# Optimization experiments

Measured on AMD Instinct MI355X. Metric: run time of the kernel, lower is better.

The kernel has to match this reference:

```python
import jax, jax.numpy as jnp
import numpy as np

GROUPS = 4
EPS = 1e-5


def conv1d(x, w, b):
    # x [B,Cin,NA,T], w [Cout,Cin,1,K], 'same' padding along T
    K = w.shape[-1]
    pad = (K - 1) // 2
    y = jax.lax.conv_general_dilated(x, w, (1, 1), [(0, 0), (pad, pad)],
                                     dimension_numbers=('NCHW', 'OIHW', 'NCHW'))
    return y + b[None, :, None, None]


def group_norm(x, g, b):
    B, C, H, W = x.shape
    xg = x.reshape(B, GROUPS, C // GROUPS, H, W)
    m = xg.mean((2, 3, 4), keepdims=True)
    v = xg.var((2, 3, 4), keepdims=True)
    xn = ((xg - m) * jax.lax.rsqrt(v + EPS)).reshape(B, C, H, W)
    return xn * g[None, :, None, None] + b[None, :, None, None]


def avg_pool_t(x, k):
    B, C, H, T = x.shape
    return x.reshape(B, C, H, T // k, k).mean(-1)


def branch(x, w1, b1, g1, be1, w2, b2, g2, be2):
    y = avg_pool_t(jax.nn.gelu(group_norm(conv1d(x, w1, b1), g1, be1), approximate=False), 2)
    y = avg_pool_t(jax.nn.gelu(group_norm(conv1d(y, w2, b2), g2, be2), approximate=False), 4)
    # B C NA T -> B NA (T C)
    B, C, NA, T = y.shape
    return jnp.transpose(y, (0, 2, 3, 1)).reshape(B, NA, T * C)


def rvq(feat, cbs):
    # feat [B,NA,D]; cbs [nq,V,D] -> residual vector quantization
    def step(res, cb):
        d = (res * res).sum(-1, keepdims=True) \
            - 2.0 * jnp.einsum('bnd,vd->bnv', res, cb) \
            + (cb * cb).sum(-1)              # [B,NA,V]
        idx = jnp.argmin(d, axis=-1)          # [B,NA]
        q = cb[idx]                           # gather [B,NA,D]
        return res - q, (q, idx)
    _, (qs, idxs) = jax.lax.scan(step, feat, cbs)
    return qs.sum(0), idxs                    # [B,NA,D], [nq,B,NA]


def reference(x, w11, w12, w13, w14, b1, g1, be1,
              w21, w22, w23, w24, b2, g2, be2, codebooks):
    B, N, A, T = x.shape
    xc = x.reshape(B, N * A, T)[:, None]  # [B,1,NA,T]
    feats = jnp.stack([
        branch(xc, w11, b1[0], g1[0], be1[0], w21, b2[0], g2[0], be2[0]),
        branch(xc, w12, b1[1], g1[1], be1[1], w22, b2[1], g2[1], be2[1]),
        branch(xc, w13, b1[2], g1[2], be1[2], w23, b2[2], g2[2], be2[2]),
        branch(xc, w14, b1[3], g1[3], be1[3], w24, b2[3], g2[3], be2[3]),
    ])  # [4,B,NA,D]
    quant, idxs = jax.vmap(rvq)(feats, codebooks)  # [4,B,NA,D], [4,nq,B,NA]
    # straight-through estimator
    out = feats + jax.lax.stop_gradient(quant - feats)
    return out, idxs


def setup_inputs() -> dict:
    key = jax.random.key(0)
    ks = jax.random.split(key, 16)
    C = 8
    d = {
        'x': jax.random.normal(ks[0], (8, 32, 4, 200), jnp.float32),
        'w11': jax.random.normal(ks[1], (C, 1, 1, 21), jnp.float32) * 0.1,
        'w12': jax.random.normal(ks[2], (C, 1, 1, 15), jnp.float32) * 0.1,
        'w13': jax.random.normal(ks[3], (C, 1, 1, 9), jnp.float32) * 0.1,
        'w14': jax.random.normal(ks[4], (C, 1, 1, 5), jnp.float32) * 0.1,
        'b1': jnp.zeros((4, C), jnp.float32),
        'g1': jnp.ones((4, C), jnp.float32),
        'be1': jnp.zeros((4, C), jnp.float32),
        'w21': jax.random.normal(ks[5], (C, C, 1, 9), jnp.float32) * 0.1,
        'w22': jax.random.normal(ks[6], (C, C, 1, 7), jnp.float32) * 0.1,
        'w23': jax.random.normal(ks[7], (C, C, 1, 5), jnp.float32) * 0.1,
        'w24': jax.random.normal(ks[8], (C, C, 1, 3), jnp.float32) * 0.1,
        'b2': jnp.zeros((4, C), jnp.float32),
        'g2': jnp.ones((4, C), jnp.float32),
        'be2': jnp.zeros((4, C), jnp.float32),
        'codebooks': jax.random.normal(ks[9], (4, 8, 8192, 200), jnp.float32) * 0.5,
    }
    return d
```

## Files before the change

kernel.cpp:

```cpp
#include <hip/hip_runtime.h>
#include <hip/hip_bf16.h>
#include <math.h>

#define NBR 4
#define BB 8
#define NAA 128
#define T_IN 200
#define CCH 8
#define NQ 8
#define NV 8192
#define DD 200
#define ROWS 1024
#define KPAD 224
#define NKG 28
#define CBQSH ((size_t)NBR*NKG*NV*8)

typedef __attribute__((ext_vector_type(8))) short short8;
typedef __attribute__((ext_vector_type(4))) float f32x4;

__device__ __forceinline__ unsigned short f2bf(float x) {
  unsigned u = __float_as_uint(x);
  unsigned r = (u + 0x7fffu + ((u >> 16) & 1u)) >> 16;
  return (unsigned short)r;
}
__device__ __forceinline__ bool lexlt(float av, int ai, float bv, int bi) {
  return (av < bv) || (av == bv && ai < bi);
}
__device__ __forceinline__ unsigned umn(unsigned a, unsigned b) { return a < b ? a : b; }
__device__ __forceinline__ unsigned umx(unsigned a, unsigned b) { return a > b ? a : b; }
__device__ __forceinline__ unsigned skey(float s, int idx) {
  unsigned u = __float_as_uint(s);
  unsigned mask = ((unsigned)((int)u >> 31)) | 0x80000000u;
  return ((u ^ mask) & 0xFFFFE000u) | (unsigned)idx;
}
__device__ __forceinline__ void gld16(const short* g, short* s) {
  __builtin_amdgcn_global_load_lds(
      (const __attribute__((address_space(1))) unsigned*)g,
      (__attribute__((address_space(3))) unsigned*)s, 16, 0, 0);
}

template<int K>
__device__ __forceinline__ void conv1_stats_body(
    const float* __restrict__ sx, const float* __restrict__ wr, float bias,
    int tl, double& s, double& s2)
{
  constexpr int pad = (K-1)/2;
  if (tl < 25) {
    int t0 = 8*tl;
    float xw[K+7];
    #pragma unroll
    for (int i = 0; i < K+7; ++i) {
      int xi = t0 - pad + i;
      xw[i] = ((unsigned)xi < (unsigned)T_IN) ? sx[xi] : 0.f;
    }
    #pragma unroll
    for (int m = 0; m < 8; ++m) {
      float acc = bias;
      #pragma unroll
      for (int k = 0; k < K; ++k)
        acc = fmaf(wr[k], xw[m + k], acc);
      s += acc; s2 += (double)acc * acc;
    }
  }
}

__global__ __launch_bounds__(256) void k_conv1_stats(
    const float* __restrict__ x,
    const float* __restrict__ w11, const float* __restrict__ w12,
    const float* __restrict__ w13, const float* __restrict__ w14,
    const float* __restrict__ b1,
    double* __restrict__ partS, double* __restrict__ partQ)
{
  const int bid = blockIdx.x;
  const int br = bid >> 10;
  const int b  = (bid >> 7) & 7;
  const int na = bid & 127;
  const int tid = threadIdx.x;
  const int c  = tid >> 5;
  const int tl = tid & 31;
  const float* w = (br==0) ? w11 : (br==1) ? w12 : (br==2) ? w13 : w14;

  __shared__ float sx[T_IN];
  if (tid < T_IN) sx[tid] = x[((size_t)b*NAA + na)*T_IN + tid];
  __syncthreads();

  const float bias = b1[br*CCH + c];
  double s = 0.0, s2 = 0.0;
  switch (br) {
    case 0: conv1_stats_body<21>(sx, w + c*21, bias, tl, s, s2); break;
    case 1: conv1_stats_body<15>(sx, w + c*15, bias, tl, s, s2); break;
    case 2: conv1_stats_body<9> (sx, w + c*9,  bias, tl, s, s2); break;
    default: conv1_stats_body<5>(sx, w + c*5,  bias, tl, s, s2); break;
  }
  __shared__ double rs[256], rq[256];
  rs[tid] = s; rq[tid] = s2;
  __syncthreads();
  for (int off = 32; off > 0; off >>= 1) {
    if ((tid & 63) < off) { rs[tid] += rs[tid+off]; rq[tid] += rq[tid+off]; }
    __syncthreads();
  }
  if ((tid & 63) == 0) {
    int g = tid >> 6;
    int pi = (((br*BB + b)*4 + g) << 7) + na;
    partS[pi] = rs[tid]; partQ[pi] = rq[tid];
  }
}

template<int K1, int K2>
__device__ __forceinline__ void mid_body(
    const float* __restrict__ sx, float* __restrict__ sy,
    const float* __restrict__ w1, const float* __restrict__ w2,
    float bias1, float fm, float rst, float gm, float bt, float bias2,
    int c, int tl, float* __restrict__ yout, double& s, double& s2)
{
  constexpr int pad1 = (K1-1)/2, pad2 = (K2-1)/2;
  const float* wr = w1 + c*K1;
  if (tl < 25) {
    int t0 = 8*tl;
    float xw[K1+7];
    #pragma unroll
    for (int i = 0; i < K1+7; ++i) {
      int xi = t0 - pad1 + i;
      xw[i] = ((unsigned)xi < (unsigned)T_IN) ? sx[xi] : 0.f;
    }
    #pragma unroll
    for (int m = 0; m < 4; ++m) {
      float u = 0.f;
      #pragma unroll
      for (int h = 0; h < 2; ++h) {
        float acc = bias1;
        #pragma unroll
        for (int k = 0; k < K1; ++k)
          acc = fmaf(wr[k], xw[2*m + h + k], acc);
        float xn = (acc - fm) * rst * gm + bt;
        u += 0.5f * xn * (1.0f + erff(xn * 0.70710678118654752440f));
      }
      sy[c*100 + 4*tl + m] = 0.5f * u;
    }
  }
  __syncthreads();
  if (tl < 25) {
    int t0 = 4*tl;
    float a0 = bias2, a1 = bias2, a2 = bias2, a3 = bias2;
    #pragma unroll
    for (int cin = 0; cin < CCH; ++cin) {
      const float* wr2 = w2 + (c*CCH + cin)*K2;
      float wv[K2];
      #pragma unroll
      for (int k = 0; k < K2; ++k) wv[k] = wr2[k];
      float yw[K2+3];
      #pragma unroll
      for (int i = 0; i < K2+3; ++i) {
        int yi = t0 - pad2 + i;
        yw[i] = ((unsigned)yi < 100u) ? sy[cin*100 + yi] : 0.f;
      }
      #pragma unroll
      for (int k = 0; k < K2; ++k) a0 = fmaf(wv[k], yw[k], a0);
      #pragma unroll
      for (int k = 0; k < K2; ++k) a1 = fmaf(wv[k], yw[1 + k], a1);
      #pragma unroll
      for (int k = 0; k < K2; ++k) a2 = fmaf(wv[k], yw[2 + k], a2);
      #pragma unroll
      for (int k = 0; k < K2; ++k) a3 = fmaf(wv[k], yw[3 + k], a3);
    }
    *(float4*)&yout[t0] = make_float4(a0, a1, a2, a3);
    s += a0; s2 += (double)a0 * a0;
    s += a1; s2 += (double)a1 * a1;
    s += a2; s2 += (double)a2 * a2;
    s += a3; s2 += (double)a3 * a3;
  }
}

__global__ __launch_bounds__(256) void k_mid(
    const float* __restrict__ x,
    const float* __restrict__ w11, const float* __restrict__ w12,
    const float* __restrict__ w13, const float* __restrict__ w14,
    const float* __restrict__ b1, const float* __restrict__ g1,
    const float* __restrict__ be1,
    const double* __restrict__ partS1, const double* __restrict__ partQ1,
    const float* __restrict__ w21, const float* __restrict__ w22,
    const float* __restrict__ w23, const float* __restrict__ w24,
    const float* __restrict__ b2,
    float* __restrict__ y2raw,
    double* __restrict__ partS, double* __restrict__ partQ)
{
  const int bid = blockIdx.x;
  const int br = bid >> 10;
  const int b  = (bid >> 7) & 7;
  const int na = bid & 127;
  const int tid = threadIdx.x;
  const int c  = tid >> 5;
  const int tl = tid & 31;
  const int wid = tid >> 6;
  const int l = tid & 63;
  const float* w1 = (br==0) ? w11 : (br==1) ? w12 : (br==2) ? w13 : w14;
  const float* w2 = (br==0) ? w21 : (br==1) ? w22 : (br==2) ? w23 : w24;

  __shared__ float sx[T_IN];
  __shared__ float sy[CCH*100];
  __shared__ float sstat[8];
  if (tid < T_IN) sx[tid] = x[((size_t)b*NAA + na)*T_IN + tid];

  {
    int base = (((br*BB + b)*4 + wid) << 7);
    double a  = partS1[base + l] + partS1[base + 64 + l];
    double qn = partQ1[base + l] + partQ1[base + 64 + l];
    #pragma unroll
    for (int m = 32; m >= 1; m >>= 1) {
      a  += __shfl_xor(a, m);
      qn += __shfl_xor(qn, m);
    }
    if (l == 0) {
      double mean = a / 51200.0;
      double var  = qn / 51200.0 - mean*mean;
      sstat[wid*2]     = (float)mean;
      sstat[wid*2 + 1] = (float)(1.0 / sqrt(var + 1e-5));
    }
  }
  __syncthreads();

  const float bias1 = b1[br*CCH + c];
  const float fm  = sstat[(c>>1)*2];
  const float rst = sstat[(c>>1)*2 + 1];
  const float gm = g1[br*CCH + c], bt = be1[br*CCH + c];
  const float bias2 = b2[br*CCH + c];
  float* yout = y2raw + ((((size_t)br*BB + b)*CCH + c)*NAA + na)*100;

  double s = 0.0, s2 = 0.0;
  switch (br) {
    case 0: mid_body<21,9>(sx, sy, w1, w2, bias1, fm, rst, gm, bt, bias2, c, tl, yout, s, s2); break;
    case 1: mid_body<15,7>(sx, sy, w1, w2, bias1, fm, rst, gm, bt, bias2, c, tl, yout, s, s2); break;
    case 2: mid_body<9,5> (sx, sy, w1, w2, bias1, fm, rst, gm, bt, bias2, c, tl, yout, s, s2); break;
    default: mid_body<5,3>(sx, sy, w1, w2, bias1, fm, rst, gm, bt, bias2, c, tl, yout, s, s2); break;
  }

  __shared__ double rs[256], rq[256];
  rs[tid] = s; rq[tid] = s2;
  __syncthreads();
  for (int off = 32; off > 0; off >>= 1) {
    if ((tid & 63) < off) { rs[tid] += rs[tid+off]; rq[tid] += rq[tid+off]; }
    __syncthreads();
  }
  if ((tid & 63) == 0) {
    int g = tid >> 6;
    int pi = (((br*BB + b)*4 + g) << 7) + na;
    partS[pi] = rs[tid]; partQ[pi] = rq[tid];
  }
}

__global__ __launch_bounds__(256) void k_tail(
    const float* __restrict__ y2raw, const float* __restrict__ g2,
    const float* __restrict__ be2,
    const double* __restrict__ partS2, const double* __restrict__ partQ2,
    float* __restrict__ res, short* __restrict__ resh)
{
  const int tid = threadIdx.x;
  int idx = blockIdx.x * 256 + tid;
  int c  = idx & 7;
  int tp = (idx >> 3) % 25;
  int na = (idx / 200) & 127;
  int b  = (idx / 25600) & 7;
  int br = idx / 204800;
  const int wid = tid >> 6, l = tid & 63;

  if (idx < NBR*3*ROWS*8) {
    int pos = idx & 7;
    int prow = (idx >> 3) & 1023;
    int r2  = idx >> 13;
    int pbr = r2 / 3, kgp = r2 - pbr*3;
    resh[(((size_t)pbr*NKG + 25 + kgp)*ROWS + prow)*8 + pos] = 0;
  }

  __shared__ float sstat[8];
  {
    int base = (((br*BB + b)*4 + wid) << 7);
    double a  = partS2[base + l] + partS2[base + 64 + l];
    double qn = partQ2[base + l] + partQ2[base + 64 + l];
    #pragma unroll
    for (int m = 32; m >= 1; m >>= 1) {
      a  += __shfl_xor(a, m);
      qn += __shfl_xor(qn, m);
    }
    if (l == 0) {
      double mean = a / 25600.0;
      double var  = qn / 25600.0 - mean*mean;
      sstat[wid*2]     = (float)mean;
      sstat[wid*2 + 1] = (float)(1.0 / sqrt(var + 1e-5));
    }
  }
  __syncthreads();

  int g = c >> 1;
  float fm  = sstat[g*2];
  float rst = sstat[g*2 + 1];
  float gm = g2[br*CCH + c], bt = be2[br*CCH + c];
  float4 v = *(const float4*)&y2raw[((((size_t)br*BB + b)*CCH + c)*NAA + na)*100 + 4*tp];
  float sum4 = 0.f;
  #pragma unroll
  for (int h = 0; h < 4; ++h) {
    float xv = (h==0) ? v.x : (h==1) ? v.y : (h==2) ? v.z : v.w;
    float xn = (xv - fm) * rst * gm + bt;
    sum4 += 0.5f * xn * (1.0f + erff(xn * 0.70710678118654752440f));
  }
  float val = 0.25f * sum4;
  int row = b*NAA + na;
  res[((size_t)br*ROWS + row)*DD + tp*8 + c] = val;
  resh[(((size_t)br*NKG + tp)*ROWS + row)*8 + c] = (short)f2bf(val);
}

__global__ __launch_bounds__(256) void k_cvt_cb(
    const float* __restrict__ cbs, int q0, int nq,
    short* __restrict__ dh, float* __restrict__ cbn)
{
  __shared__ short S[25][65][8];
  const int blk = blockIdx.x;
  const int vt = blk & 127;
  const int t  = blk >> 7;
  const int br = t / nq, ql = t - br*nq;
  const int q = q0 + ql;
  const int tid = threadIdx.x;
  const int row = tid >> 2, fq = tid & 3;
  const int v0 = vt*64;
  const float* srow = cbs + ((size_t)(br*NQ + q)*NV + v0 + row)*DD;

  float s = 0.f;
  for (int j = 0; j < 13; ++j) {
    int f4 = fq + 4*j;
    if (f4 < 50) {
      float4 f = *(const float4*)&srow[4*f4];
      s += f.x*f.x + f.y*f.y + f.z*f.z + f.w*f.w;
      *(short4*)&S[f4>>1][row][(f4&1)*4] =
          make_short4((short)f2bf(f.x), (short)f2bf(f.y),
                      (short)f2bf(f.z), (short)f2bf(f.w));
    }
  }
  s += __shfl_xor(s, 1);
  s += __shfl_xor(s, 2);
  if (fq == 0) cbn[(size_t)(br*NQ + q)*NV + v0 + row] = s;
  __syncthreads();

  short* dq = dh + (size_t)ql*CBQSH;
  for (int u = tid; u < NKG*64*2; u += 256) {
    int kg = u >> 7;
    int rem = u & 127;
    int v = rem >> 1, pos = (rem & 1)*4;
    short4 val = (kg < 25) ? *(const short4*)&S[kg][v][pos]
                           : make_short4(0,0,0,0);
    *(short4*)&dq[(((size_t)br*NKG + kg)*NV + v0 + v)*8 + pos] = val;
  }
}

__global__ __launch_bounds__(256) void k_gemm(
    const short* __restrict__ resh, const short* __restrict__ cbh,
    const float* __restrict__ cbn, int q,
    unsigned* __restrict__ candk)
{
  __shared__ short S[2][4][128][8];

  const int p = blockIdx.x;
  const int x = p & 7;
  const int sIdx = p >> 3;
  const int br = sIdx >> 6;
  const int rb = (sIdx >> 3) & 7;
  const int vb = x*8 + (sIdx & 7);
  const int tid = threadIdx.x;
  const int w = tid >> 6;
  const int l = tid & 63;
  const int wr = w >> 1, wc = w & 1;
  const int kgl = l >> 4, fr = l & 15;

  f32x4 acc[4][4];
  #pragma unroll
  for (int i = 0; i < 4; ++i)
    #pragma unroll
    for (int j = 0; j < 4; ++j)
      acc[i][j] = (f32x4){0.f, 0.f, 0.f, 0.f};

  short8 aA[2][4];

  #define STAGE(nb, ks)                                                         \
    {                                                                           \
      _Pragma("unroll")                                                         \
      for (int i = 0; i < 4; ++i)                                               \
        aA[nb][i] = *(const short8*)&resh[                                      \
          (((size_t)br*NKG + (ks)*4 + kgl)*ROWS + rb*128 + wr*64 + i*16 + fr)*8]; \
      _Pragma("unroll")                                                         \
      for (int t = 0; t < 2; ++t) {                                             \
        int u = (w << 1) | t;                                                   \
        int kg = u >> 1, wh = u & 1;                                            \
        gld16(cbh + (((size_t)br*NKG + (ks)*4 + kg)*NV + vb*128 + wh*64 + l)*8, \
              &S[nb][kg][wh*64][0]);                                            \
      }                                                                         \
    }

  STAGE(0, 0);

  #pragma unroll
  for (int ks = 0; ks < 7; ++ks) {
    const int cur = ks & 1, nxt = cur ^ 1;
    if (ks < 6) {
      STAGE(nxt, ks + 1);
      asm volatile("s_waitcnt vmcnt(6)" ::: "memory");
    } else {
      asm volatile("s_waitcnt vmcnt(0)" ::: "memory");
    }
    __builtin_amdgcn_s_barrier();

    short8 bh[4];
    #pragma unroll
    for (int j = 0; j < 4; ++j)
      bh[j] = *(const short8*)&S[cur][kgl][wc*64 + j*16 + fr][0];
    #pragma unroll
    for (int i = 0; i < 4; ++i)
      #pragma unroll
      for (int j = 0; j < 4; ++j)
        acc[i][j] = __builtin_amdgcn_mfma_f32_16x16x32_bf16(aA[cur][i], bh[j], acc[i][j], 0, 0, 0);

    asm volatile("" ::: "memory");
    __builtin_amdgcn_s_barrier();
  }

  const float* cn = cbn + (size_t)(br*NQ + q)*NV;
  float nj[4]; int vgj[4];
  #pragma unroll
  for (int j = 0; j < 4; ++j) {
    vgj[j] = vb*128 + wc*64 + j*16 + fr;
    nj[j] = 0.5f * cn[vgj[j]];
  }
  #pragma unroll
  for (int i = 0; i < 4; ++i) {
    #pragma unroll
    for (int reg = 0; reg < 4; ++reg) {
      unsigned k0 = skey(nj[0] - acc[i][0][reg], vgj[0]);
      unsigned k1 = skey(nj[1] - acc[i][1][reg], vgj[1]);
      unsigned k2 = skey(nj[2] - acc[i][2][reg], vgj[2]);
      unsigned k3 = skey(nj[3] - acc[i][3][reg], vgj[3]);
      unsigned a = umn(k0, k1), b = umx(k0, k1);
      unsigned c = umn(k2, k3), d = umx(k2, k3);
      unsigned c1 = umn(a, c);
      unsigned c2 = umn(umx(a, c), umn(b, d));
      #pragma unroll
      for (int m = 1; m <= 8; m <<= 1) {
        unsigned o1 = __shfl_xor(c1, m);
        unsigned o2 = __shfl_xor(c2, m);
        unsigned t = umx(c1, o1);
        c1 = umn(c1, o1);
        c2 = umn(umn(t, c2), o2);
      }
      if (fr == 0) {
        int grow = br*ROWS + rb*128 + wr*64 + i*16 + kgl*4 + reg;
        size_t o = ((size_t)grow*64 + vb)*4 + wc*2;
        candk[o] = c1; candk[o+1] = c2;
      }
    }
  }
  #undef STAGE
}

__global__ __launch_bounds__(256) void k_update3(
    const float* __restrict__ cbs, const float* __restrict__ cbn,
    const unsigned* __restrict__ candk,
    float* __restrict__ res, float* __restrict__ outq,
    float* __restrict__ outi, short* __restrict__ resh, int q)
{
  const int wid = threadIdx.x >> 6;
  const int lane = threadIdx.x & 63;
  const int r = blockIdx.x*4 + wid;
  const int br = r >> 10;
  const int row = r & 1023;

  const unsigned* ck = candk + (size_t)r * 256;
  uint4 kk = *(const uint4*)&ck[4*lane];
  unsigned c0 = kk.x, c1 = kk.y, c2 = kk.z, c3 = kk.w;

  unsigned mykey = 0xFFFFFFFFu;
  #pragma unroll
  for (int t = 0; t < 8; ++t) {
    unsigned lm = umn(umn(c0, c1), umn(c2, c3));
    #pragma unroll
    for (int m = 1; m <= 32; m <<= 1)
      lm = umn(lm, __shfl_xor(lm, m));
    if (c0 == lm) c0 = 0xFFFFFFFFu;
    if (c1 == lm) c1 = 0xFFFFFFFFu;
    if (c2 == lm) c2 = 0xFFFFFFFFu;
    if (c3 == lm) c3 = 0xFFFFFFFFu;
    if ((lane >> 3) == t) mykey = lm;
  }
  const int mycand = (int)(mykey & 0x1FFFu);

  const int kl = lane & 7;
  const float* cbrow = cbs + ((size_t)(br*NQ + q)*NV + mycand)*DD;
  const float* rrow0 = res + (size_t)r*DD;
  float dot = 0.f;
  #pragma unroll
  for (int u = 0; u < 7; ++u) {
    int f4 = kl + 8*u;
    if (f4 < 50) {
      float4 r4 = *(const float4*)&rrow0[4*f4];
      float4 c4 = *(const float4*)&cbrow[4*f4];
      dot = fmaf(r4.x, c4.x, dot);
      dot = fmaf(r4.y, c4.y, dot);
      dot = fmaf(r4.z, c4.z, dot);
      dot = fmaf(r4.w, c4.w, dot);
    }
  }
  dot += __shfl_xor(dot, 1);
  dot += __shfl_xor(dot, 2);
  dot += __shfl_xor(dot, 4);
  float dist = fmaf(-2.f, dot, cbn[(size_t)(br*NQ + q)*NV + mycand]);

  float bv = dist; int bi = mycand;
  #pragma unroll
  for (int m = 8; m <= 32; m <<= 1) {
    float ov = __shfl_xor(bv, m); int oi = __shfl_xor(bi, m);
    if (lexlt(ov, oi, bv, bi)) { bv = ov; bi = oi; }
  }

  if (lane == 0)
    outi[(((size_t)br*NQ + q)*BB + (row >> 7))*NAA + (row & 127)] = (float)bi;

  const float* c = cbs + ((size_t)(br*NQ + q)*NV + bi)*DD;
  float* rrow = res  + ((size_t)br*ROWS + row)*DD;
  float* qrow = outq + ((size_t)br*ROWS + row)*DD;
  if (lane < 50) {
    float4 cvv = *(const float4*)&c[4*lane];
    float4 r4 = *(const float4*)&rrow[4*lane];
    r4.x -= cvv.x; r4.y -= cvv.y; r4.z -= cvv.z; r4.w -= cvv.w;
    *(float4*)&rrow[4*lane] = r4;
    float4 qv;
    if (q == 0) {
      qv = cvv;
    } else {
      qv = *(const float4*)&qrow[4*lane];
      qv.x += cvv.x; qv.y += cvv.y; qv.z += cvv.z; qv.w += cvv.w;
    }
    *(float4*)&qrow[4*lane] = qv;

    *(short4*)&resh[(((size_t)br*NKG + (lane>>1))*ROWS + row)*8 + (lane&1)*4] =
        make_short4((short)f2bf(r4.x), (short)f2bf(r4.y),
                    (short)f2bf(r4.z), (short)f2bf(r4.w));
  }
}

extern "C" void kernel_launch(void* const* d_in, const int* in_sizes, int n_in,
                              void* d_out, int out_size, void* d_ws, size_t ws_size,
                              hipStream_t stream)
{
  const float* x   = (const float*)d_in[0];
  const float* w11 = (const float*)d_in[1];
  const float* w12 = (const float*)d_in[2];
  const float* w13 = (const float*)d_in[3];
  const float* w14 = (const float*)d_in[4];
  const float* b1  = (const float*)d_in[5];
  const float* g1  = (const float*)d_in[6];
  const float* be1 = (const float*)d_in[7];
  const float* w21 = (const float*)d_in[8];
  const float* w22 = (const float*)d_in[9];
  const float* w23 = (const float*)d_in[10];
  const float* w24 = (const float*)d_in[11];
  const float* b2  = (const float*)d_in[12];
  const float* g2  = (const float*)d_in[13];
  const float* be2 = (const float*)d_in[14];
  const float* cbs = (const float*)d_in[15];

  char* wsb = (char*)d_ws;
  double* partS1 = (double*)wsb;
  double* partQ1 = partS1 + 16384;
  double* partS2 = partQ1 + 16384;
  double* partQ2 = partS2 + 16384;
  float* fbase = (float*)(partQ2 + 16384);
  float* y2raw = fbase + 512;
  float* res   = y2raw + 3276800;
  float* cbn   = res + 819200;
  unsigned* candk = (unsigned*)(cbn + 262144);
  short* resh  = (short*)(candk + 1048576);
  short* cbh   = resh + 917504;
  const size_t base_bytes = (char*)cbh - wsb;
  const bool big = ws_size >= base_bytes + CBQSH*8*sizeof(short) + 1024;

  float* outq = (float*)d_out;
  float* outi = outq + 819200;

  k_conv1_stats<<<4096, 256, 0, stream>>>(x, w11, w12, w13, w14, b1, partS1, partQ1);
  k_mid<<<4096, 256, 0, stream>>>(x, w11, w12, w13, w14, b1, g1, be1,
                                  partS1, partQ1,
                                  w21, w22, w23, w24, b2, y2raw, partS2, partQ2);
  k_tail<<<3200, 256, 0, stream>>>(y2raw, g2, be2, partS2, partQ2, res, resh);

  if (big)
    k_cvt_cb<<<NBR*NQ*128, 256, 0, stream>>>(cbs, 0, NQ, cbh, cbn);

  for (int q = 0; q < NQ; ++q) {
    if (!big)
      k_cvt_cb<<<NBR*128, 256, 0, stream>>>(cbs, q, 1, cbh, cbn);
    const short* cbh_q = cbh + (big ? (size_t)q*CBQSH : 0);
    k_gemm<<<2048, 256, 0, stream>>>(resh, cbh_q, cbn, q, candk);
    k_update3<<<1024, 256, 0, stream>>>(cbs, cbn, candk, res, outq, outi,
                                        resh, q);
  }
}
```

Before: 427.3 us.

## Fuse codebook bf16 conversion into GEMM with LDS-resident codebook tile

Removes the separate codebook conversion kernel and its bf16 global buffer. Each GEMM block now loads a 128-entry fp32 codebook tile, converts it to bf16 in LDS, computes the codebook norms there, and reuses the tile across four row blocks, so the grid shrinks from 2048 to 512 blocks. The update kernel recomputes the exact distance as c·(c-2r) instead of reading stored norms. In exchange the per-block LDS footprint and serial work grow, the grid is smaller, and the double-buffered async LDS pipeline is gone. Norms used for candidate selection now come from bf16-rounded values, and a redundant dead LDS load was left in the inner loop.

```diff
diff --git a/kernel.cpp b/kernel.cpp
--- a/kernel.cpp
+++ b/kernel.cpp
@@ -13,7 +13,6 @@
 #define ROWS 1024
 #define KPAD 224
 #define NKG 28
-#define CBQSH ((size_t)NBR*NKG*NV*8)
 
 typedef __attribute__((ext_vector_type(8))) short short8;
 typedef __attribute__((ext_vector_type(4))) float f32x4;
@@ -22,6 +21,9 @@
   unsigned u = __float_as_uint(x);
   unsigned r = (u + 0x7fffu + ((u >> 16) & 1u)) >> 16;
   return (unsigned short)r;
+}
+__device__ __forceinline__ float bf2f(short h) {
+  return __uint_as_float(((unsigned)(unsigned short)h) << 16);
 }
 __device__ __forceinline__ bool lexlt(float av, int ai, float bv, int bi) {
   return (av < bv) || (av == bv && ai < bi);
@@ -32,11 +34,6 @@
   unsigned u = __float_as_uint(s);
   unsigned mask = ((unsigned)((int)u >> 31)) | 0x80000000u;
   return ((u ^ mask) & 0xFFFFE000u) | (unsigned)idx;
-}
-__device__ __forceinline__ void gld16(const short* g, short* s) {
-  __builtin_amdgcn_global_load_lds(
-      (const __attribute__((address_space(1))) unsigned*)g,
-      (__attribute__((address_space(3))) unsigned*)s, 16, 0, 0);
 }
 
 template<int K>
@@ -308,157 +305,140 @@
   resh[(((size_t)br*NKG + tp)*ROWS + row)*8 + c] = (short)f2bf(val);
 }
 
-__global__ __launch_bounds__(256) void k_cvt_cb(
-    const float* __restrict__ cbs, int q0, int nq,
-    short* __restrict__ dh, float* __restrict__ cbn)
-{
-  __shared__ short S[25][65][8];
-  const int blk = blockIdx.x;
-  const int vt = blk & 127;
-  const int t  = blk >> 7;
-  const int br = t / nq, ql = t - br*nq;
-  const int q = q0 + ql;
-  const int tid = threadIdx.x;
-  const int row = tid >> 2, fq = tid & 3;
-  const int v0 = vt*64;
-  const float* srow = cbs + ((size_t)(br*NQ + q)*NV + v0 + row)*DD;
-
-  float s = 0.f;
-  for (int j = 0; j < 13; ++j) {
-    int f4 = fq + 4*j;
-    if (f4 < 50) {
-      float4 f = *(const float4*)&srow[4*f4];
-      s += f.x*f.x + f.y*f.y + f.z*f.z + f.w*f.w;
-      *(short4*)&S[f4>>1][row][(f4&1)*4] =
-          make_short4((short)f2bf(f.x), (short)f2bf(f.y),
-                      (short)f2bf(f.z), (short)f2bf(f.w));
-    }
-  }
-  s += __shfl_xor(s, 1);
-  s += __shfl_xor(s, 2);
-  if (fq == 0) cbn[(size_t)(br*NQ + q)*NV + v0 + row] = s;
-  __syncthreads();
-
-  short* dq = dh + (size_t)ql*CBQSH;
-  for (int u = tid; u < NKG*64*2; u += 256) {
-    int kg = u >> 7;
-    int rem = u & 127;
-    int v = rem >> 1, pos = (rem & 1)*4;
-    short4 val = (kg < 25) ? *(const short4*)&S[kg][v][pos]
-                           : make_short4(0,0,0,0);
-    *(short4*)&dq[(((size_t)br*NKG + kg)*NV + v0 + v)*8 + pos] = val;
-  }
-}
-
 __global__ __launch_bounds__(256) void k_gemm(
-    const short* __restrict__ resh, const short* __restrict__ cbh,
-    const float* __restrict__ cbn, int q,
+    const short* __restrict__ resh, const float* __restrict__ cbs, int q,
     unsigned* __restrict__ candk)
 {
-  __shared__ short S[2][4][128][8];
+  __shared__ short B[NKG][130][8];
+  __shared__ float nrm[128];
 
   const int p = blockIdx.x;
-  const int x = p & 7;
+  const int xcd = p & 7;
   const int sIdx = p >> 3;
-  const int br = sIdx >> 6;
-  const int rb = (sIdx >> 3) & 7;
-  const int vb = x*8 + (sIdx & 7);
+  const int rbh = sIdx & 1;
+  const int vb  = xcd*8 + ((sIdx >> 1) & 7);
+  const int br  = sIdx >> 4;
   const int tid = threadIdx.x;
   const int w = tid >> 6;
   const int l = tid & 63;
   const int wr = w >> 1, wc = w & 1;
   const int kgl = l >> 4, fr = l & 15;
 
-  f32x4 acc[4][4];
-  #pragma unroll
-  for (int i = 0; i < 4; ++i)
-    #pragma unroll
-    for (int j = 0; j < 4; ++j)
-      acc[i][j] = (f32x4){0.f, 0.f, 0.f, 0.f};
-
-  short8 aA[2][4];
-
-  #define STAGE(nb, ks)                                                         \
-    {                                                                           \
-      _Pragma("unroll")                                                         \
-      for (int i = 0; i < 4; ++i)                                               \
-        aA[nb][i] = *(const short8*)&resh[                                      \
-          (((size_t)br*NKG + (ks)*4 + kgl)*ROWS + rb*128 + wr*64 + i*16 + fr)*8]; \
-      _Pragma("unroll")                                                         \
-      for (int t = 0; t < 2; ++t) {                                             \
-        int u = (w << 1) | t;                                                   \
-        int kg = u >> 1, wh = u & 1;                                            \
-        gld16(cbh + (((size_t)br*NKG + (ks)*4 + kg)*NV + vb*128 + wh*64 + l)*8, \
-              &S[nb][kg][wh*64][0]);                                            \
-      }                                                                         \
-    }
-
-  STAGE(0, 0);
-
-  #pragma unroll
-  for (int ks = 0; ks < 7; ++ks) {
-    const int cur = ks & 1, nxt = cur ^ 1;
-    if (ks < 6) {
-      STAGE(nxt, ks + 1);
-      asm volatile("s_waitcnt vmcnt(6)" ::: "memory");
-    } else {
-      asm volatile("s_waitcnt vmcnt(0)" ::: "memory");
-    }
-    __builtin_amdgcn_s_barrier();
-
-    short8 bh[4];
-    #pragma unroll
-    for (int j = 0; j < 4; ++j)
-      bh[j] = *(const short8*)&S[cur][kgl][wc*64 + j*16 + fr][0];
+  const float* cbbase = cbs + ((size_t)(br*NQ + q)*NV + (size_t)vb*128)*DD;
+  for (int i = 0; i < 13; ++i) {
+    int u = tid + 256*i;
+    if (u < 3200) {
+      int v = u / 25, kg = u - v*25;
+      const float* sp = cbbase + (size_t)v*DD + kg*8;
+      float4 f0 = *(const float4*)sp;
+      float4 f1 = *(const float4*)(sp + 4);
+      short8 o;
+      o[0]=(short)f2bf(f0.x); o[1]=(short)f2bf(f0.y);
+      o[2]=(short)f2bf(f0.z); o[3]=(short)f2bf(f0.w);
+      o[4]=(short)f2bf(f1.x); o[5]=(short)f2bf(f1.y);
+      o[6]=(short)f2bf(f1.z); o[7]=(short)f2bf(f1.w);
+      *(short8*)&B[kg][v][0] = o;
+    }
+  }
+  for (int z = tid; z < 3*130*4; z += 256)
+    ((int*)&B[25][0][0])[z] = 0;
+  __syncthreads();
+
+  {
+    int v = tid >> 1, half = tid & 1;
+    float sq = 0.f;
+    int kg0 = half ? 13 : 0, kg1 = half ? 25 : 13;
+    for (int kg = kg0; kg < kg1; ++kg) {
+      short8 sv = *(const short8*)&B[kg][v][0];
+      #pragma unroll
+      for (int j = 0; j < 8; ++j) {
+        float c = bf2f(sv[j]);
+        sq = fmaf(c, c, sq);
+      }
+    }
+    sq += __shfl_xor(sq, 1);
+    if (half == 0) nrm[v] = sq;
+  }
+  __syncthreads();
+
+  for (int r4 = 0; r4 < 4; ++r4) {
+    const int rb = rbh*4 + r4;
+
+    f32x4 acc[4][4];
     #pragma unroll
     for (int i = 0; i < 4; ++i)
       #pragma unroll
       for (int j = 0; j < 4; ++j)
-        acc[i][j] = __builtin_amdgcn_mfma_f32_16x16x32_bf16(aA[cur][i], bh[j], acc[i][j], 0, 0, 0);
-
-    asm volatile("" ::: "memory");
-    __builtin_amdgcn_s_barrier();
-  }
-
-  const float* cn = cbn + (size_t)(br*NQ + q)*NV;
-  float nj[4]; int vgj[4];
-  #pragma unroll
-  for (int j = 0; j < 4; ++j) {
-    vgj[j] = vb*128 + wc*64 + j*16 + fr;
-    nj[j] = 0.5f * cn[vgj[j]];
-  }
-  #pragma unroll
-  for (int i = 0; i < 4; ++i) {
-    #pragma unroll
-    for (int reg = 0; reg < 4; ++reg) {
-      unsigned k0 = skey(nj[0] - acc[i][0][reg], vgj[0]);
-      unsigned k1 = skey(nj[1] - acc[i][1][reg], vgj[1]);
-      unsigned k2 = skey(nj[2] - acc[i][2][reg], vgj[2]);
-      unsigned k3 = skey(nj[3] - acc[i][3][reg], vgj[3]);
-      unsigned a = umn(k0, k1), b = umx(k0, k1);
-      unsigned c = umn(k2, k3), d = umx(k2, k3);
-      unsigned c1 = umn(a, c);
-      unsigned c2 = umn(umx(a, c), umn(b, d));
-      #pragma unroll
-      for (int m = 1; m <= 8; m <<= 1) {
-        unsigned o1 = __shfl_xor(c1, m);
-        unsigned o2 = __shfl_xor(c2, m);
-        unsigned t = umx(c1, o1);
-        c1 = umn(c1, o1);
-        c2 = umn(umn(t, c2), o2);
+        acc[i][j] = (f32x4){0.f, 0.f, 0.f, 0.f};
+
+    short8 aA[2][4];
+    #define LOAD_A(nb, ks)                                                        \
+      {                                                                           \
+        _Pragma("unroll")                                                         \
+        for (int i = 0; i < 4; ++i)                                               \
+          aA[nb][i] = *(const short8*)&resh[                                      \
+            (((size_t)br*NKG + (ks)*4 + kgl)*ROWS + rb*128 + wr*64 + i*16 + fr)*8]; \
       }
-      if (fr == 0) {
-        int grow = br*ROWS + rb*128 + wr*64 + i*16 + kgl*4 + reg;
-        size_t o = ((size_t)grow*64 + vb)*4 + wc*2;
-        candk[o] = c1; candk[o+1] = c2;
+
+    LOAD_A(0, 0);
+    #pragma unroll
+    for (int ks = 0; ks < 7; ++ks) {
+      const int cur = ks & 1, nxt = cur ^ 1;
+      if (ks < 6) LOAD_A(nxt, ks + 1);
+      short8 bh[4];
+      #pragma unroll
+      for (int j = 0; j < 4; ++j)
+        bh[j] = *(const short8*)&B[kgl*4 + ks - kgl*4 + 0][0][0];
+      #pragma unroll
+      for (int j = 0; j < 4; ++j)
+        bh[j] = *(const short8*)&B[ks*4 + kgl][wc*64 + j*16 + fr][0];
+      #pragma unroll
+      for (int i = 0; i < 4; ++i)
+        #pragma unroll
+        for (int j = 0; j < 4; ++j)
+          acc[i][j] = __builtin_amdgcn_mfma_f32_16x16x32_bf16(aA[cur][i], bh[j], acc[i][j], 0, 0, 0);
+    }
+    #undef LOAD_A
+
+    float nj[4]; int vgj[4];
+    #pragma unroll
+    for (int j = 0; j < 4; ++j) {
+      int lv = wc*64 + j*16 + fr;
+      vgj[j] = vb*128 + lv;
+      nj[j] = 0.5f * nrm[lv];
+    }
+    #pragma unroll
+    for (int i = 0; i < 4; ++i) {
+      #pragma unroll
+      for (int reg = 0; reg < 4; ++reg) {
+        unsigned k0 = skey(nj[0] - acc[i][0][reg], vgj[0]);
+        unsigned k1 = skey(nj[1] - acc[i][1][reg], vgj[1]);
+        unsigned k2 = skey(nj[2] - acc[i][2][reg], vgj[2]);
+        unsigned k3 = skey(nj[3] - acc[i][3][reg], vgj[3]);
+        unsigned a = umn(k0, k1), b = umx(k0, k1);
+        unsigned c = umn(k2, k3), d = umx(k2, k3);
+        unsigned c1 = umn(a, c);
+        unsigned c2 = umn(umx(a, c), umn(b, d));
+        #pragma unroll
+        for (int m = 1; m <= 8; m <<= 1) {
+          unsigned o1 = __shfl_xor(c1, m);
+          unsigned o2 = __shfl_xor(c2, m);
+          unsigned t = umx(c1, o1);
+          c1 = umn(c1, o1);
+          c2 = umn(umn(t, c2), o2);
+        }
+        if (fr == 0) {
+          int grow = br*ROWS + rb*128 + wr*64 + i*16 + kgl*4 + reg;
+          size_t o = ((size_t)grow*64 + vb)*4 + wc*2;
+          candk[o] = c1; candk[o+1] = c2;
+        }
       }
     }
   }
-  #undef STAGE
 }
 
 __global__ __launch_bounds__(256) void k_update3(
-    const float* __restrict__ cbs, const float* __restrict__ cbn,
+    const float* __restrict__ cbs,
     const unsigned* __restrict__ candk,
     float* __restrict__ res, float* __restrict__ outq,
     float* __restrict__ outi, short* __restrict__ resh, int q)
@@ -491,23 +471,23 @@
   const int kl = lane & 7;
   const float* cbrow = cbs + ((size_t)(br*NQ + q)*NV + mycand)*DD;
   const float* rrow0 = res + (size_t)r*DD;
-  float dot = 0.f;
+  float e = 0.f;
   #pragma unroll
   for (int u = 0; u < 7; ++u) {
     int f4 = kl + 8*u;
     if (f4 < 50) {
       float4 r4 = *(const float4*)&rrow0[4*f4];
       float4 c4 = *(const float4*)&cbrow[4*f4];
-      dot = fmaf(r4.x, c4.x, dot);
-      dot = fmaf(r4.y, c4.y, dot);
-      dot = fmaf(r4.z, c4.z, dot);
-      dot = fmaf(r4.w, c4.w, dot);
-    }
-  }
-  dot += __shfl_xor(dot, 1);
-  dot += __shfl_xor(dot, 2);
-  dot += __shfl_xor(dot, 4);
-  float dist = fmaf(-2.f, dot, cbn[(size_t)(br*NQ + q)*NV + mycand]);
+      e = fmaf(c4.x, fmaf(-2.f, r4.x, c4.x), e);
+      e = fmaf(c4.y, fmaf(-2.f, r4.y, c4.y), e);
+      e = fmaf(c4.z, fmaf(-2.f, r4.z, c4.z), e);
+      e = fmaf(c4.w, fmaf(-2.f, r4.w, c4.w), e);
+    }
+  }
+  e += __shfl_xor(e, 1);
+  e += __shfl_xor(e, 2);
+  e += __shfl_xor(e, 4);
+  float dist = e;
 
   float bv = dist; int bi = mycand;
   #pragma unroll
@@ -569,14 +549,10 @@
   double* partS2 = partQ1 + 16384;
   double* partQ2 = partS2 + 16384;
   float* fbase = (float*)(partQ2 + 16384);
-  float* y2raw = fbase + 512;
+  float* y2raw = fbase;
   float* res   = y2raw + 3276800;
-  float* cbn   = res + 819200;
-  unsigned* candk = (unsigned*)(cbn + 262144);
+  unsigned* candk = (unsigned*)(res + 819200);
   short* resh  = (short*)(candk + 1048576);
-  short* cbh   = resh + 917504;
-  const size_t base_bytes = (char*)cbh - wsb;
-  const bool big = ws_size >= base_bytes + CBQSH*8*sizeof(short) + 1024;
 
   float* outq = (float*)d_out;
   float* outi = outq + 819200;
@@ -587,15 +563,8 @@
                                   w21, w22, w23, w24, b2, y2raw, partS2, partQ2);
   k_tail<<<3200, 256, 0, stream>>>(y2raw, g2, be2, partS2, partQ2, res, resh);
 
-  if (big)
-    k_cvt_cb<<<NBR*NQ*128, 256, 0, stream>>>(cbs, 0, NQ, cbh, cbn);
-
   for (int q = 0; q < NQ; ++q) {
-    if (!big)
-      k_cvt_cb<<<NBR*128, 256, 0, stream>>>(cbs, q, 1, cbh, cbn);
-    const short* cbh_q = cbh + (big ? (size_t)q*CBQSH : 0);
-    k_gemm<<<2048, 256, 0, stream>>>(resh, cbh_q, cbn, q, candk);
-    k_update3<<<1024, 256, 0, stream>>>(cbs, cbn, candk, res, outq, outi,
-                                        resh, q);
-  }
-}
+    k_gemm<<<512, 256, 0, stream>>>(resh, cbs, q, candk);
+    k_update3<<<1024, 256, 0, stream>>>(cbs, candk, res, outq, outi, resh, q);
+  }
+}
```

Result: slower. 461.5 us (+8.0%).

## Keep full codebook tile resident in LDS and loop over row blocks in GEMM

Applied to the files above, without the earlier changes.

The GEMM kernel now loads the entire K extent of a 128-entry codebook tile into shared memory once. It then iterates over four 128-row blocks of residuals, which cuts the grid from 2048 to 512 blocks and cuts repeated codebook loads. Residual fragments still stream from global memory with double buffering, and the per-stage barriers are gone. The rerank kernel now computes the distance as c·(c−2r) directly instead of reading the precomputed norm. The trade-offs are larger LDS use per block (about 58 KB), lower occupancy and fewer blocks in the grid.

```diff
diff --git a/kernel.cpp b/kernel.cpp
--- a/kernel.cpp
+++ b/kernel.cpp
@@ -355,70 +355,28 @@
     const float* __restrict__ cbn, int q,
     unsigned* __restrict__ candk)
 {
-  __shared__ short S[2][4][128][8];
+  __shared__ short B[NKG][130][8];
 
   const int p = blockIdx.x;
-  const int x = p & 7;
+  const int xcd = p & 7;
   const int sIdx = p >> 3;
-  const int br = sIdx >> 6;
-  const int rb = (sIdx >> 3) & 7;
-  const int vb = x*8 + (sIdx & 7);
+  const int rbh = sIdx & 1;
+  const int vb  = xcd*8 + ((sIdx >> 1) & 7);
+  const int br  = sIdx >> 4;
   const int tid = threadIdx.x;
   const int w = tid >> 6;
   const int l = tid & 63;
   const int wr = w >> 1, wc = w & 1;
   const int kgl = l >> 4, fr = l & 15;
 
-  f32x4 acc[4][4];
   #pragma unroll
-  for (int i = 0; i < 4; ++i)
-    #pragma unroll
-    for (int j = 0; j < 4; ++j)
-      acc[i][j] = (f32x4){0.f, 0.f, 0.f, 0.f};
-
-  short8 aA[2][4];
-
-  #define STAGE(nb, ks)                                                         \
-    {                                                                           \
-      _Pragma("unroll")                                                         \
-      for (int i = 0; i < 4; ++i)                                               \
-        aA[nb][i] = *(const short8*)&resh[                                      \
-          (((size_t)br*NKG + (ks)*4 + kgl)*ROWS + rb*128 + wr*64 + i*16 + fr)*8]; \
-      _Pragma("unroll")                                                         \
-      for (int t = 0; t < 2; ++t) {                                             \
-        int u = (w << 1) | t;                                                   \
-        int kg = u >> 1, wh = u & 1;                                            \
-        gld16(cbh + (((size_t)br*NKG + (ks)*4 + kg)*NV + vb*128 + wh*64 + l)*8, \
-              &S[nb][kg][wh*64][0]);                                            \
-      }                                                                         \
-    }
-
-  STAGE(0, 0);
-
-  #pragma unroll
-  for (int ks = 0; ks < 7; ++ks) {
-    const int cur = ks & 1, nxt = cur ^ 1;
-    if (ks < 6) {
-      STAGE(nxt, ks + 1);
-      asm volatile("s_waitcnt vmcnt(6)" ::: "memory");
-    } else {
-      asm volatile("s_waitcnt vmcnt(0)" ::: "memory");
-    }
-    __builtin_amdgcn_s_barrier();
-
-    short8 bh[4];
-    #pragma unroll
-    for (int j = 0; j < 4; ++j)
-      bh[j] = *(const short8*)&S[cur][kgl][wc*64 + j*16 + fr][0];
-    #pragma unroll
-    for (int i = 0; i < 4; ++i)
-      #pragma unroll
-      for (int j = 0; j < 4; ++j)
-        acc[i][j] = __builtin_amdgcn_mfma_f32_16x16x32_bf16(aA[cur][i], bh[j], acc[i][j], 0, 0, 0);
-
-    asm volatile("" ::: "memory");
-    __builtin_amdgcn_s_barrier();
-  }
+  for (int t = 0; t < 14; ++t) {
+    int u = w*14 + t;
+    int kg = u >> 1, wh = u & 1;
+    gld16(cbh + (((size_t)br*NKG + kg)*NV + (size_t)vb*128 + wh*64 + l)*8,
+          &B[kg][wh*64][0]);
+  }
+  __syncthreads();
 
   const float* cn = cbn + (size_t)(br*NQ + q)*NV;
   float nj[4]; int vgj[4];
@@ -427,38 +385,76 @@
     vgj[j] = vb*128 + wc*64 + j*16 + fr;
     nj[j] = 0.5f * cn[vgj[j]];
   }
-  #pragma unroll
-  for (int i = 0; i < 4; ++i) {
-    #pragma unroll
-    for (int reg = 0; reg < 4; ++reg) {
-      unsigned k0 = skey(nj[0] - acc[i][0][reg], vgj[0]);
-      unsigned k1 = skey(nj[1] - acc[i][1][reg], vgj[1]);
-      unsigned k2 = skey(nj[2] - acc[i][2][reg], vgj[2]);
-      unsigned k3 = skey(nj[3] - acc[i][3][reg], vgj[3]);
-      unsigned a = umn(k0, k1), b = umx(k0, k1);
-      unsigned c = umn(k2, k3), d = umx(k2, k3);
-      unsigned c1 = umn(a, c);
-      unsigned c2 = umn(umx(a, c), umn(b, d));
-      #pragma unroll
-      for (int m = 1; m <= 8; m <<= 1) {
-        unsigned o1 = __shfl_xor(c1, m);
-        unsigned o2 = __shfl_xor(c2, m);
-        unsigned t = umx(c1, o1);
-        c1 = umn(c1, o1);
-        c2 = umn(umn(t, c2), o2);
+
+  #pragma unroll 1
+  for (int r4 = 0; r4 < 4; ++r4) {
+    const int rb = rbh*4 + r4;
+
+    f32x4 acc[4][4];
+    #pragma unroll
+    for (int i = 0; i < 4; ++i)
+      #pragma unroll
+      for (int j = 0; j < 4; ++j)
+        acc[i][j] = (f32x4){0.f, 0.f, 0.f, 0.f};
+
+    short8 aA[2][4];
+    #define LOAD_A(nb, ks)                                                        \
+      {                                                                           \
+        _Pragma("unroll")                                                         \
+        for (int i = 0; i < 4; ++i)                                               \
+          aA[nb][i] = *(const short8*)&resh[                                      \
+            (((size_t)br*NKG + (ks)*4 + kgl)*ROWS + rb*128 + wr*64 + i*16 + fr)*8]; \
       }
-      if (fr == 0) {
-        int grow = br*ROWS + rb*128 + wr*64 + i*16 + kgl*4 + reg;
-        size_t o = ((size_t)grow*64 + vb)*4 + wc*2;
-        candk[o] = c1; candk[o+1] = c2;
+
+    LOAD_A(0, 0);
+    #pragma unroll
+    for (int ks = 0; ks < 7; ++ks) {
+      const int cur = ks & 1, nxt = cur ^ 1;
+      if (ks < 6) LOAD_A(nxt, ks + 1);
+      short8 bh[4];
+      #pragma unroll
+      for (int j = 0; j < 4; ++j)
+        bh[j] = *(const short8*)&B[ks*4 + kgl][wc*64 + j*16 + fr][0];
+      #pragma unroll
+      for (int i = 0; i < 4; ++i)
+        #pragma unroll
+        for (int j = 0; j < 4; ++j)
+          acc[i][j] = __builtin_amdgcn_mfma_f32_16x16x32_bf16(aA[cur][i], bh[j], acc[i][j], 0, 0, 0);
+    }
+    #undef LOAD_A
+
+    #pragma unroll
+    for (int i = 0; i < 4; ++i) {
+      #pragma unroll
+      for (int reg = 0; reg < 4; ++reg) {
+        unsigned k0 = skey(nj[0] - acc[i][0][reg], vgj[0]);
+        unsigned k1 = skey(nj[1] - acc[i][1][reg], vgj[1]);
+        unsigned k2 = skey(nj[2] - acc[i][2][reg], vgj[2]);
+        unsigned k3 = skey(nj[3] - acc[i][3][reg], vgj[3]);
+        unsigned a = umn(k0, k1), b = umx(k0, k1);
+        unsigned c = umn(k2, k3), d = umx(k2, k3);
+        unsigned c1 = umn(a, c);
+        unsigned c2 = umn(umx(a, c), umn(b, d));
+        #pragma unroll
+        for (int m = 1; m <= 8; m <<= 1) {
+          unsigned o1 = __shfl_xor(c1, m);
+          unsigned o2 = __shfl_xor(c2, m);
+          unsigned t = umx(c1, o1);
+          c1 = umn(c1, o1);
+          c2 = umn(umn(t, c2), o2);
+        }
+        if (fr == 0) {
+          int grow = br*ROWS + rb*128 + wr*64 + i*16 + kgl*4 + reg;
+          size_t o = ((size_t)grow*64 + vb)*4 + wc*2;
+          candk[o] = c1; candk[o+1] = c2;
+        }
       }
     }
   }
-  #undef STAGE
 }
 
 __global__ __launch_bounds__(256) void k_update3(
-    const float* __restrict__ cbs, const float* __restrict__ cbn,
+    const float* __restrict__ cbs,
     const unsigned* __restrict__ candk,
     float* __restrict__ res, float* __restrict__ outq,
     float* __restrict__ outi, short* __restrict__ resh, int q)
@@ -491,23 +487,23 @@
   const int kl = lane & 7;
   const float* cbrow = cbs + ((size_t)(br*NQ + q)*NV + mycand)*DD;
   const float* rrow0 = res + (size_t)r*DD;
-  float dot = 0.f;
+  float e = 0.f;
   #pragma unroll
   for (int u = 0; u < 7; ++u) {
     int f4 = kl + 8*u;
     if (f4 < 50) {
       float4 r4 = *(const float4*)&rrow0[4*f4];
       float4 c4 = *(const float4*)&cbrow[4*f4];
-      dot = fmaf(r4.x, c4.x, dot);
-      dot = fmaf(r4.y, c4.y, dot);
-      dot = fmaf(r4.z, c4.z, dot);
-      dot = fmaf(r4.w, c4.w, dot);
-    }
-  }
-  dot += __shfl_xor(dot, 1);
-  dot += __shfl_xor(dot, 2);
-  dot += __shfl_xor(dot, 4);
-  float dist = fmaf(-2.f, dot, cbn[(size_t)(br*NQ + q)*NV + mycand]);
+      e = fmaf(c4.x, fmaf(-2.f, r4.x, c4.x), e);
+      e = fmaf(c4.y, fmaf(-2.f, r4.y, c4.y), e);
+      e = fmaf(c4.z, fmaf(-2.f, r4.z, c4.z), e);
+      e = fmaf(c4.w, fmaf(-2.f, r4.w, c4.w), e);
+    }
+  }
+  e += __shfl_xor(e, 1);
+  e += __shfl_xor(e, 2);
+  e += __shfl_xor(e, 4);
+  float dist = e;
 
   float bv = dist; int bi = mycand;
   #pragma unroll
@@ -569,7 +565,7 @@
   double* partS2 = partQ1 + 16384;
   double* partQ2 = partS2 + 16384;
   float* fbase = (float*)(partQ2 + 16384);
-  float* y2raw = fbase + 512;
+  float* y2raw = fbase;
   float* res   = y2raw + 3276800;
   float* cbn   = res + 819200;
   unsigned* candk = (unsigned*)(cbn + 262144);
@@ -594,8 +590,7 @@
     if (!big)
       k_cvt_cb<<<NBR*128, 256, 0, stream>>>(cbs, q, 1, cbh, cbn);
     const short* cbh_q = cbh + (big ? (size_t)q*CBQSH : 0);
-    k_gemm<<<2048, 256, 0, stream>>>(resh, cbh_q, cbn, q, candk);
-    k_update3<<<1024, 256, 0, stream>>>(cbs, cbn, candk, res, outq, outi,
-                                        resh, q);
-  }
-}
+    k_gemm<<<512, 256, 0, stream>>>(resh, cbh_q, cbn, q, candk);
+    k_update3<<<1024, 256, 0, stream>>>(cbs, candk, res, outq, outi, resh, q);
+  }
+}
```

New measurement: 497.7 us. 1.16x slower.
